# Kernel optimization log

Measured on AMD Instinct MI355X. Metric: run time of the kernel, lower is better.

## Reference

```python
import jax, jax.numpy as jnp
import numpy as np

B, C, D, E = 2048, 64, 1024, 128
P_INT = 0.0  # p_int=0 -> intervention mask is all zeros (deterministic)


def setup_inputs() -> dict:
    key = jax.random.key(0)
    ks = jax.random.split(key, 16)
    s = lambda k, shape, fan: jax.random.normal(k, shape, jnp.float32) * (1.0 / np.sqrt(fan))
    return {
        "x": jax.random.normal(ks[0], (B, D), jnp.float32),
        "c_int": jax.random.uniform(ks[1], (B, C), jnp.float32),
        # stacked per-concept scorer MLP: Linear(D,D) -> ReLU -> Linear(D,1) -> Sigmoid
        "W1": s(ks[2], (C, D, D), D), "b1": jnp.zeros((C, D), jnp.float32),
        "w2": s(ks[3], (C, D), D), "b2": jnp.zeros((C,), jnp.float32),
        # stacked per-concept embed layer: Linear(D+1, D+1) -> ReLU
        "Wl": s(ks[4], (C, D + 1, D + 1), D + 1), "bl": jnp.zeros((C, D + 1), jnp.float32),
        # shared heads
        "Wmu": s(ks[5], (D + 1, E), D + 1), "bmu": jnp.zeros((E,), jnp.float32),
        "Wlv": s(ks[6], (D + 1, E), D + 1), "blv": jnp.zeros((E,), jnp.float32),
        "proto_pos": jax.random.normal(ks[7], (C, E), jnp.float32),
        "proto_neg": jax.random.normal(ks[8], (C, E), jnp.float32),
    }


def reference(x, c_int, W1, b1, w2, b2, Wl, bl, Wmu, bmu, Wlv, blv, proto_pos, proto_neg):
    # Concept scorers (all concepts batched as one grouped GEMM).
    h = jax.nn.relu(jnp.einsum("bd,cdk->bck", x, W1) + b1)          # [B,C,D]
    c_pred = jax.nn.sigmoid(jnp.einsum("bck,ck->bc", h, w2) + b2)    # [B,C]
    # Per-concept embedding layer on [x ; c_pred].
    xc = jnp.concatenate(
        [jnp.broadcast_to(x[:, None, :], (x.shape[0], C, D)), c_pred[..., None]], axis=-1
    )                                                                # [B,C,D+1]
    emb = jax.nn.relu(jnp.einsum("bck,ckj->bcj", xc, Wl) + bl)       # [B,C,D+1]
    mu = jnp.einsum("bcj,je->bce", emb, Wmu) + bmu                   # [B,C,E]
    logvar = jnp.einsum("bcj,je->bce", emb, Wlv) + blv               # [B,C,E]
    c_emb = mu  # eval mode: no reparameterization noise
    # Intervention blend (mask ~ Bernoulli(p_int); p_int=0 -> zeros, deterministic)
    mask = jnp.zeros_like(c_pred)                                    # [B,C]
    cp = mask * c_int + (1.0 - mask) * c_pred                        # [B,C]
    proto = cp[..., None] * proto_pos + (1.0 - cp[..., None]) * proto_neg  # [B,C,E]
    c_emb = mask[..., None] * proto + (1.0 - mask[..., None]) * c_emb
    return (c_pred, c_emb, mu, logvar)
```

## Files before the change

kernel.cpp:

```cpp
#include <hip/hip_runtime.h>
#include <hip/hip_bf16.h>
#include <cstdint>
#include <cstddef>

#define OFF_CE 131072ull
#define OFF_MU (131072ull + 16777216ull)
#define OFF_LV (131072ull + 33554432ull)

using bf16x8 = __attribute__((ext_vector_type(8))) __bf16;
using s16x8  = __attribute__((ext_vector_type(8))) short;
using f32x4  = __attribute__((ext_vector_type(4))) float;

__device__ __forceinline__ unsigned short f2bf(float x) {
  unsigned u = __builtin_bit_cast(unsigned, x);
  return (unsigned short)((u + 0x7FFFu + ((u >> 16) & 1u)) >> 16);
}
__device__ __forceinline__ float bf2f(unsigned short h) {
  unsigned u = ((unsigned)h) << 16;
  return __builtin_bit_cast(float, u);
}
__device__ __forceinline__ void async16(const void* g, void* l) {
  __builtin_amdgcn_global_load_lds(
      (const __attribute__((address_space(1))) void*)g,
      (__attribute__((address_space(3))) void*)l, 16, 0, 0);
}


__global__ __launch_bounds__(256) void convert_x_k(const float* __restrict__ x,
                                                   unsigned short* __restrict__ xb) {
  int idx = blockIdx.x * 256 + threadIdx.x;
  const float4* xv = (const float4*)x;
  float4 a = xv[idx * 2], b = xv[idx * 2 + 1];
  unsigned w0 = f2bf(a.x) | ((unsigned)f2bf(a.y) << 16);
  unsigned w1 = f2bf(a.z) | ((unsigned)f2bf(a.w) << 16);
  unsigned w2 = f2bf(b.x) | ((unsigned)f2bf(b.y) << 16);
  unsigned w3 = f2bf(b.z) | ((unsigned)f2bf(b.w) << 16);
  ((uint4*)xb)[idx] = make_uint4(w0, w1, w2, w3);
}

__global__ void transpose_w1_k(const float* __restrict__ src0, unsigned short* __restrict__ dst0) {
  __shared__ float t[32][33];
  const int c = blockIdx.z;
  const int k0 = blockIdx.x << 5, n0 = blockIdx.y << 5;
  const int tx = threadIdx.x, ty = threadIdx.y;
  const float* src = src0 + ((size_t)c << 20);
#pragma unroll
  for (int r = 0; r < 4; ++r)
    t[ty + (r << 3)][tx] = src[((size_t)(k0 + ty + (r << 3)) << 10) + n0 + tx];
  __syncthreads();
  unsigned short* dst = dst0 + ((size_t)c << 20);
#pragma unroll
  for (int r = 0; r < 4; ++r)
    dst[((size_t)(n0 + ty + (r << 3)) << 10) + k0 + tx] = f2bf(t[tx][ty + (r << 3)]);
}

__global__ void transpose_wl_k(const float* __restrict__ Wl, unsigned short* __restrict__ WlT) {
  __shared__ float t[32][33];
  const int c = blockIdx.z;
  const int k0 = blockIdx.x << 5, n0 = blockIdx.y << 5;
  const int tx = threadIdx.x, ty = threadIdx.y;
  const float* src = Wl + (size_t)c * 1025 * 1025;
#pragma unroll
  for (int r = 0; r < 4; ++r)
    t[ty + (r << 3)][tx] = src[(size_t)(k0 + ty + (r << 3)) * 1025 + n0 + tx];
  __syncthreads();
  unsigned short* dst = WlT + ((size_t)c << 20);
#pragma unroll
  for (int r = 0; r < 4; ++r)
    dst[((size_t)(n0 + ty + (r << 3)) << 10) + k0 + tx] = f2bf(t[tx][ty + (r << 3)]);
}

__global__ __launch_bounds__(256) void prep_wl_k(const float* __restrict__ Wl,
                                                 const float* __restrict__ bl,
                                                 float* __restrict__ wlastf,
                                                 float* __restrict__ blpf,
                                                 float* __restrict__ Wlcolf,
                                                 float* __restrict__ w2l,
                                                 float* __restrict__ bl1024) {
  int idx = blockIdx.x * 256 + threadIdx.x;
  int c = idx >> 10, j = idx & 1023;
  const float* src = Wl + (size_t)c * 1025 * 1025;
  wlastf[idx] = src[(size_t)1024 * 1025 + j];
  blpf[idx]   = bl[(size_t)c * 1025 + j];
  Wlcolf[idx] = src[(size_t)j * 1025 + 1024];
  if (j == 0) {
    w2l[c]    = src[(size_t)1024 * 1025 + 1024];
    bl1024[c] = bl[(size_t)c * 1025 + 1024];
  }
}

__global__ __launch_bounds__(256) void convert_whead_k(const float* __restrict__ Wmu,
                                                       const float* __restrict__ Wlv,
                                                       unsigned short* __restrict__ WheadT,
                                                       float* __restrict__ whead1024f) {
  int idx = blockIdx.x * 256 + threadIdx.x;
  int rr = idx >> 10, k = idx & 1023;
  float v = (rr < 128) ? Wmu[(size_t)k * 128 + rr] : Wlv[(size_t)k * 128 + (rr - 128)];
  WheadT[idx] = f2bf(v);
  if (blockIdx.x == 0 && threadIdx.x < 256) {
    int r2 = threadIdx.x;
    whead1024f[r2] = (r2 < 128) ? Wmu[(size_t)1024 * 128 + r2] : Wlv[(size_t)1024 * 128 + (r2 - 128)];
  }
}

__global__ __launch_bounds__(256) void colgemv_k(const unsigned short* __restrict__ xb,
                                                 const float* __restrict__ Wlcolf,
                                                 float* __restrict__ presum) {
  __shared__ unsigned short xt[32 * 1024];
  const int r0 = blockIdx.x << 5;
  const int tid = threadIdx.x;
#pragma unroll
  for (int i = 0; i < 16; ++i)
    ((uint4*)xt)[tid * 16 + i] = ((const uint4*)(xb + (size_t)r0 * 1024))[tid * 16 + i];
  __syncthreads();
  const int wv = tid >> 6, lane = tid & 63;
  for (int c = 0; c < 64; ++c) {
    float4 w[4];
#pragma unroll
    for (int q = 0; q < 4; ++q)
      w[q] = *(const float4*)(Wlcolf + (c << 10) + lane * 16 + q * 4);
#pragma unroll
    for (int rr = 0; rr < 8; ++rr) {
      const int r = (wv << 3) + rr;
      const unsigned short* xr = xt + (r << 10) + lane * 16;
      s16x8 h0 = *(const s16x8*)xr;
      s16x8 h1 = *(const s16x8*)(xr + 8);
      float s = 0.f;
#pragma unroll
      for (int i = 0; i < 8; ++i) {
        s += bf2f((unsigned short)h0[i]) * ((const float*)&w[i >> 2])[i & 3];
        s += bf2f((unsigned short)h1[i]) * ((const float*)&w[2 + (i >> 2)])[i & 3];
      }
#pragma unroll
      for (int off = 32; off; off >>= 1) s += __shfl_xor(s, off);
      if (lane == 0) presum[(c << 11) + r0 + r] = s;
    }
  }
}

__global__ __launch_bounds__(256) void sigmoid_k(const float* __restrict__ spart,
                                                 const float* __restrict__ b2,
                                                 const float* __restrict__ presum,
                                                 const float* __restrict__ w2l,
                                                 const float* __restrict__ bl1024,
                                                 float* __restrict__ pred_out,
                                                 float* __restrict__ cpf,
                                                 float* __restrict__ e1024f) {
  int idx = blockIdx.x * 256 + threadIdx.x;
  int b = idx >> 6, c = idx & 63;
  float s = b2[c];
#pragma unroll
  for (int q = 0; q < 4; ++q) s += spart[(((size_t)(q << 6) + c) << 11) + b];
  float p = 1.f / (1.f + expf(-s));
  pred_out[idx] = p;
  cpf[idx] = p;
  e1024f[(c << 11) + b] = fmaxf(presum[(c << 11) + b] + p * w2l[c] + bl1024[c], 0.f);
}


#define BAR() __builtin_amdgcn_s_barrier()
#define LGKM0() do { asm volatile("s_waitcnt lgkmcnt(0)" ::: "memory"); \
                     __builtin_amdgcn_sched_barrier(0); } while (0)
#define VM4() asm volatile("s_waitcnt vmcnt(4)" ::: "memory")
#define VM0() asm volatile("s_waitcnt vmcnt(0)" ::: "memory")

#define STAGEA(h, tt, bidx) do { _Pragma("unroll") for (int q_ = 0; q_ < 2; ++q_) \
  async16(Asrc[q_] + ((size_t)(h) * 128) * K + (size_t)(tt) * 64, \
          &sA[bidx][(h) * 8192 + chnk[q_]]); } while (0)
#define STAGEB(h, tt, bidx) do { _Pragma("unroll") for (int q_ = 0; q_ < 2; ++q_) \
  async16(Bsrc[q_] + ((size_t)(h) * 128) * K + (size_t)(tt) * 64, \
          &sB[bidx][(h) * 8192 + chnk[q_]]); } while (0)

#define LOADA(mh, bidx) do { _Pragma("unroll") for (int i_ = 0; i_ < 4; ++i_) { \
  const int ro_ = ((mh) * 128 + wm64 + i_ * 16 + l15) << 6; \
  a[i_][0] = *(const bf16x8*)&sA[bidx][ro_ + ccx0]; \
  a[i_][1] = *(const bf16x8*)&sA[bidx][ro_ + ccx1]; } } while (0)

#define LOADB(nh, bb, bidx) do { _Pragma("unroll") for (int j_ = 0; j_ < 2; ++j_) { \
  const int ro_ = ((nh) * 128 + wn32 + j_ * 16 + l15) << 6; \
  bb[j_][0] = *(const bf16x8*)&sB[bidx][ro_ + ccx0]; \
  bb[j_][1] = *(const bf16x8*)&sB[bidx][ro_ + ccx1]; } } while (0)

#define MMAQ(mh, nh, bb) do { _Pragma("unroll") for (int i_ = 0; i_ < 4; ++i_) \
  _Pragma("unroll") for (int j_ = 0; j_ < 2; ++j_) { \
    acc[(mh)*4+i_][(nh)*2+j_] = __builtin_amdgcn_mfma_f32_16x16x32_bf16( \
        a[i_][0], bb[j_][0], acc[(mh)*4+i_][(nh)*2+j_], 0, 0, 0); \
    acc[(mh)*4+i_][(nh)*2+j_] = __builtin_amdgcn_mfma_f32_16x16x32_bf16( \
        a[i_][1], bb[j_][1], acc[(mh)*4+i_][(nh)*2+j_], 0, 0, 0); \
  } } while (0)

template <int MODE>
__global__ __launch_bounds__(512, 2) void gemm8p_k(
    const unsigned short* __restrict__ A, const unsigned short* __restrict__ BT, const int K,
    const float* __restrict__ e0, const float* __restrict__ e1,
    const float* __restrict__ e2, const float* __restrict__ e3,
    unsigned short* __restrict__ obf, float* __restrict__ ofl) {
  __shared__ unsigned short sA[2][16384];
  __shared__ unsigned short sB[2][16384];

  constexpr int GX = (MODE == 2) ? 1 : 4;
  constexpr int GY = (MODE == 2) ? 512 : 8;
  constexpr int NWG = GX * GY * ((MODE == 2) ? 1 : 64);

  const int tid = threadIdx.x;
  const int lane = tid & 63;
  const int wid = tid >> 6;
  const int wm = wid >> 2, wn = wid & 3;
  const int l15 = lane & 15, l4 = lane >> 4;
  const int wm64 = wm << 6, wn32 = wn << 5;

  const int rbid = blockIdx.x + GX * (blockIdx.y + GY * blockIdx.z);
  const int bid = (rbid & 7) * (NWG >> 3) + (rbid >> 3);
  const int bx = bid % GX;
  const int by = (bid / GX) % GY;
  const int c = bid / (GX * GY);

  const int n0 = bx << 8;
  const int m0 = by << 8;

  const unsigned short* Ab = A;
  const unsigned short* Bb;
  if constexpr (MODE == 2) Bb = BT;
  else                     Bb = BT + ((size_t)c << 20);

  int rloc[2], csrc[2], chnk[2];
  const unsigned short* Asrc[2];
  const unsigned short* Bsrc[2];
#pragma unroll
  for (int q = 0; q < 2; ++q) {
    const int s = ((wid << 1) + q) * 64 + lane;
    rloc[q] = s >> 3;
    csrc[q] = ((s & 7) ^ ((s >> 3) & 7)) << 3;
    chnk[q] = ((wid << 1) + q) << 9;
    Asrc[q] = Ab + (size_t)(m0 + rloc[q]) * K + csrc[q];
    Bsrc[q] = Bb + (size_t)(n0 + rloc[q]) * K + csrc[q];
  }

  const int xorv = l15 & 7;
  const int ccx0 = (l4 ^ xorv) << 3;
  const int ccx1 = ((4 + l4) ^ xorv) << 3;

  f32x4 acc[8][4];
#pragma unroll
  for (int i = 0; i < 8; ++i)
#pragma unroll
    for (int j = 0; j < 4; ++j) acc[i][j] = (f32x4)(0.f);

  bf16x8 a[4][2], b0[2][2], b1[2][2];

  const int nt = K >> 6;

  STAGEA(0, 0, 0); STAGEB(0, 0, 0); STAGEB(1, 0, 0); STAGEA(1, 0, 0);
  VM0();
  BAR();

  for (int t = 0; t < nt - 1; ++t) {
    const int cb = t & 1, nb = cb ^ 1;
    LOADA(0, cb);
    LOADB(0, b0, cb);
    STAGEA(0, t + 1, nb);
    BAR();
    LGKM0();
    __builtin_amdgcn_s_setprio(1);
    MMAQ(0, 0, b0);
    __builtin_amdgcn_s_setprio(0);
    VM4();
    BAR();
    LOADB(1, b1, cb);
    STAGEB(0, t + 1, nb);
    BAR();
    LGKM0();
    __builtin_amdgcn_s_setprio(1);
    MMAQ(0, 1, b1);
    __builtin_amdgcn_s_setprio(0);
    VM4();
    BAR();
    LOADA(1, cb);
    STAGEB(1, t + 1, nb);
    BAR();
    LGKM0();
    __builtin_amdgcn_s_setprio(1);
    MMAQ(1, 1, b1);
    __builtin_amdgcn_s_setprio(0);
    BAR();
    STAGEA(1, t + 1, nb);
    BAR();
    __builtin_amdgcn_s_setprio(1);
    MMAQ(1, 0, b0);
    __builtin_amdgcn_s_setprio(0);
    VM4();
    BAR();
  }

  {
    const int cb = (nt - 1) & 1;
    VM0();
    BAR();
    LOADA(0, cb);
    LOADB(0, b0, cb);
    LGKM0();
    __builtin_amdgcn_s_setprio(1);
    MMAQ(0, 0, b0);
    __builtin_amdgcn_s_setprio(0);
    LOADB(1, b1, cb);
    LGKM0();
    __builtin_amdgcn_s_setprio(1);
    MMAQ(0, 1, b1);
    __builtin_amdgcn_s_setprio(0);
    LOADA(1, cb);
    LGKM0();
    __builtin_amdgcn_s_setprio(1);
    MMAQ(1, 1, b1);
    MMAQ(1, 0, b0);
    __builtin_amdgcn_s_setprio(0);
  }

  int coln[2][2];
#pragma unroll
  for (int nh = 0; nh < 2; ++nh)
#pragma unroll
    for (int j = 0; j < 2; ++j) coln[nh][j] = n0 + nh * 128 + wn32 + j * 16 + l15;

  if constexpr (MODE == 0) {
    float bias[2][2], w2v[2][2];
#pragma unroll
    for (int nh = 0; nh < 2; ++nh)
#pragma unroll
      for (int j = 0; j < 2; ++j) {
        bias[nh][j] = e0[(c << 10) + coln[nh][j]];
        w2v[nh][j]  = e1[(c << 10) + coln[nh][j]];
      }
    float* partL = (float*)&sA[0][0];
#pragma unroll
    for (int mh = 0; mh < 2; ++mh)
#pragma unroll
      for (int i = 0; i < 4; ++i)
#pragma unroll
        for (int rr = 0; rr < 4; ++rr) {
          float s = 0.f;
#pragma unroll
          for (int nh = 0; nh < 2; ++nh)
#pragma unroll
            for (int j = 0; j < 2; ++j) {
              float v = fmaxf(acc[mh * 4 + i][nh * 2 + j][rr] + bias[nh][j], 0.f);
              s += v * w2v[nh][j];
            }
          s += __shfl_xor(s, 1); s += __shfl_xor(s, 2);
          s += __shfl_xor(s, 4); s += __shfl_xor(s, 8);
          if (l15 == 0) partL[wid * 128 + mh * 64 + i * 16 + (l4 << 2) + rr] = s;
        }
    __syncthreads();
    if (tid < 256) {
      const int r = tid;
      const int mh_ = r >> 7, wmr = (r >> 6) & 1, low = r & 63;
      float s2 = 0.f;
#pragma unroll
      for (int wn2 = 0; wn2 < 4; ++wn2) s2 += partL[(wmr * 4 + wn2) * 128 + mh_ * 64 + low];
      ofl[(((size_t)(bx << 6) + c) << 11) + m0 + r] = s2;
    }
  } else if constexpr (MODE == 1) {
    float wl4[2][2], bb4[2][2];
#pragma unroll
    for (int nh = 0; nh < 2; ++nh)
#pragma unroll
      for (int j = 0; j < 2; ++j) {
        wl4[nh][j] = e0[(c << 10) + coln[nh][j]];
        bb4[nh][j] = e1[(c << 10) + coln[nh][j]];
      }
#pragma unroll
    for (int mh = 0; mh < 2; ++mh)
#pragma unroll
      for (int i = 0; i < 4; ++i)
#pragma unroll
        for (int rr = 0; rr < 4; ++rr) {
          const int row = m0 + mh * 128 + wm64 + i * 16 + (l4 << 2) + rr;
          const float cp = e2[((size_t)row << 6) + c];
          unsigned short* orow = obf + (((size_t)(c << 11) + row) << 10);
#pragma unroll
          for (int nh = 0; nh < 2; ++nh)
#pragma unroll
            for (int j = 0; j < 2; ++j) {
              float v = acc[mh * 4 + i][nh * 2 + j][rr] + cp * wl4[nh][j] + bb4[nh][j];
              orow[coln[nh][j]] = f2bf(fmaxf(v, 0.f));
            }
        }
  } else {
    float bias[2][2], wh[2][2];
#pragma unroll
    for (int nh = 0; nh < 2; ++nh)
#pragma unroll
      for (int j = 0; j < 2; ++j) {
        bias[nh][j] = (nh == 0) ? e0[coln[0][j]] : e1[coln[1][j] - 128];
        wh[nh][j]   = e3[coln[nh][j]];
      }
#pragma unroll
    for (int mh = 0; mh < 2; ++mh)
#pragma unroll
      for (int i = 0; i < 4; ++i)
#pragma unroll
        for (int rr = 0; rr < 4; ++rr) {
          const int rid = m0 + mh * 128 + wm64 + i * 16 + (l4 << 2) + rr;
          const int cc = rid >> 11, b = rid & 2047;
          const float ev = e2[rid];
          const size_t ib = (((size_t)b << 6) + cc) << 7;
#pragma unroll
          for (int j = 0; j < 2; ++j) {
            float v = acc[mh * 4 + i][j][rr] + bias[0][j] + ev * wh[0][j];
            ofl[OFF_MU + ib + coln[0][j]] = v;
            ofl[OFF_CE + ib + coln[0][j]] = v;
          }
#pragma unroll
          for (int j = 0; j < 2; ++j) {
            float v = acc[mh * 4 + i][2 + j][rr] + bias[1][j] + ev * wh[1][j];
            ofl[OFF_LV + ib + (coln[1][j] - 128)] = v;
          }
        }
  }
}


extern "C" void kernel_launch(void* const* d_in, const int* in_sizes, int n_in,
                              void* d_out, int out_size, void* d_ws, size_t ws_size,
                              hipStream_t stream) {
  const float* x   = (const float*)d_in[0];
  const float* W1  = (const float*)d_in[2];
  const float* b1  = (const float*)d_in[3];
  const float* w2  = (const float*)d_in[4];
  const float* b2  = (const float*)d_in[5];
  const float* Wl  = (const float*)d_in[6];
  const float* bl  = (const float*)d_in[7];
  const float* Wmu = (const float*)d_in[8];
  const float* bmu = (const float*)d_in[9];
  const float* Wlv = (const float*)d_in[10];
  const float* blv = (const float*)d_in[11];
  float* out = (float*)d_out;

  char* ws = (char*)d_ws;
  unsigned short* xb     = (unsigned short*)(ws);
  unsigned short* WT     = (unsigned short*)(ws + 4194304ull);
  float* wlastf          = (float*)(ws + 138412032ull);
  float* blpf            = (float*)(ws + 138674176ull);
  float* Wlcolf          = (float*)(ws + 138936320ull);
  float* w2l             = (float*)(ws + 139198464ull);
  float* bl1024          = (float*)(ws + 139198720ull);
  unsigned short* WheadT = (unsigned short*)(ws + 139198976ull);
  float* whead1024f      = (float*)(ws + 139723264ull);
  float* presum          = (float*)(ws + 139724288ull);
  float* spart           = (float*)(ws + 140248576ull);
  float* cpf             = (float*)(ws + 142345728ull);
  float* e1024f          = (float*)(ws + 142870016ull);
  unsigned short* emb    = (unsigned short*)(ws + 143394304ull);

  convert_x_k<<<1024, 256, 0, stream>>>(x, xb);
  transpose_w1_k<<<dim3(32, 32, 64), dim3(32, 8), 0, stream>>>(W1, WT);
  prep_wl_k<<<256, 256, 0, stream>>>(Wl, bl, wlastf, blpf, Wlcolf, w2l, bl1024);
  convert_whead_k<<<1024, 256, 0, stream>>>(Wmu, Wlv, WheadT, whead1024f);
  colgemv_k<<<64, 256, 0, stream>>>(xb, Wlcolf, presum);
  gemm8p_k<0><<<dim3(4, 8, 64), 512, 0, stream>>>(xb, WT, 1024, b1, w2, nullptr, nullptr,
                                                  nullptr, spart);
  sigmoid_k<<<512, 256, 0, stream>>>(spart, b2, presum, w2l, bl1024, out, cpf, e1024f);
  transpose_wl_k<<<dim3(32, 32, 64), dim3(32, 8), 0, stream>>>(Wl, WT);
  gemm8p_k<1><<<dim3(4, 8, 64), 512, 0, stream>>>(xb, WT, 1024, wlastf, blpf, cpf, nullptr,
                                                  emb, nullptr);
  gemm8p_k<2><<<dim3(1, 512, 1), 512, 0, stream>>>(emb, WheadT, 1024, bmu, blv, e1024f,
                                                   whead1024f, nullptr, out);
}
```

Before: 1.117 ms.

## Fuse prep kernels and overlap weight transposes with the first grouped GEMM

```diff
diff --git a/kernel.cpp b/kernel.cpp
--- a/kernel.cpp
+++ b/kernel.cpp
@@ -25,136 +25,127 @@
       (__attribute__((address_space(3))) void*)l, 16, 0, 0);
 }
 
-
-__global__ __launch_bounds__(256) void convert_x_k(const float* __restrict__ x,
-                                                   unsigned short* __restrict__ xb) {
-  int idx = blockIdx.x * 256 + threadIdx.x;
-  const float4* xv = (const float4*)x;
-  float4 a = xv[idx * 2], b = xv[idx * 2 + 1];
-  unsigned w0 = f2bf(a.x) | ((unsigned)f2bf(a.y) << 16);
-  unsigned w1 = f2bf(a.z) | ((unsigned)f2bf(a.w) << 16);
-  unsigned w2 = f2bf(b.x) | ((unsigned)f2bf(b.y) << 16);
-  unsigned w3 = f2bf(b.z) | ((unsigned)f2bf(b.w) << 16);
-  ((uint4*)xb)[idx] = make_uint4(w0, w1, w2, w3);
-}
-
-__global__ void transpose_w1_k(const float* __restrict__ src0, unsigned short* __restrict__ dst0) {
-  __shared__ float t[32][33];
-  const int c = blockIdx.z;
-  const int k0 = blockIdx.x << 5, n0 = blockIdx.y << 5;
-  const int tx = threadIdx.x, ty = threadIdx.y;
-  const float* src = src0 + ((size_t)c << 20);
-#pragma unroll
-  for (int r = 0; r < 4; ++r)
-    t[ty + (r << 3)][tx] = src[((size_t)(k0 + ty + (r << 3)) << 10) + n0 + tx];
-  __syncthreads();
-  unsigned short* dst = dst0 + ((size_t)c << 20);
-#pragma unroll
-  for (int r = 0; r < 4; ++r)
-    dst[((size_t)(n0 + ty + (r << 3)) << 10) + k0 + tx] = f2bf(t[tx][ty + (r << 3)]);
-}
-
-__global__ void transpose_wl_k(const float* __restrict__ Wl, unsigned short* __restrict__ WlT) {
-  __shared__ float t[32][33];
-  const int c = blockIdx.z;
-  const int k0 = blockIdx.x << 5, n0 = blockIdx.y << 5;
-  const int tx = threadIdx.x, ty = threadIdx.y;
-  const float* src = Wl + (size_t)c * 1025 * 1025;
-#pragma unroll
-  for (int r = 0; r < 4; ++r)
-    t[ty + (r << 3)][tx] = src[(size_t)(k0 + ty + (r << 3)) * 1025 + n0 + tx];
-  __syncthreads();
-  unsigned short* dst = WlT + ((size_t)c << 20);
-#pragma unroll
-  for (int r = 0; r < 4; ++r)
-    dst[((size_t)(n0 + ty + (r << 3)) << 10) + k0 + tx] = f2bf(t[tx][ty + (r << 3)]);
-}
-
-__global__ __launch_bounds__(256) void prep_wl_k(const float* __restrict__ Wl,
-                                                 const float* __restrict__ bl,
-                                                 float* __restrict__ wlastf,
-                                                 float* __restrict__ blpf,
-                                                 float* __restrict__ Wlcolf,
-                                                 float* __restrict__ w2l,
-                                                 float* __restrict__ bl1024) {
-  int idx = blockIdx.x * 256 + threadIdx.x;
-  int c = idx >> 10, j = idx & 1023;
-  const float* src = Wl + (size_t)c * 1025 * 1025;
-  wlastf[idx] = src[(size_t)1024 * 1025 + j];
-  blpf[idx]   = bl[(size_t)c * 1025 + j];
-  Wlcolf[idx] = src[(size_t)j * 1025 + 1024];
-  if (j == 0) {
-    w2l[c]    = src[(size_t)1024 * 1025 + 1024];
-    bl1024[c] = bl[(size_t)c * 1025 + 1024];
-  }
-}
-
-__global__ __launch_bounds__(256) void convert_whead_k(const float* __restrict__ Wmu,
-                                                       const float* __restrict__ Wlv,
-                                                       unsigned short* __restrict__ WheadT,
-                                                       float* __restrict__ whead1024f) {
-  int idx = blockIdx.x * 256 + threadIdx.x;
-  int rr = idx >> 10, k = idx & 1023;
-  float v = (rr < 128) ? Wmu[(size_t)k * 128 + rr] : Wlv[(size_t)k * 128 + (rr - 128)];
-  WheadT[idx] = f2bf(v);
-  if (blockIdx.x == 0 && threadIdx.x < 256) {
-    int r2 = threadIdx.x;
-    whead1024f[r2] = (r2 < 128) ? Wmu[(size_t)1024 * 128 + r2] : Wlv[(size_t)1024 * 128 + (r2 - 128)];
-  }
-}
-
-__global__ __launch_bounds__(256) void colgemv_k(const unsigned short* __restrict__ xb,
-                                                 const float* __restrict__ Wlcolf,
-                                                 float* __restrict__ presum) {
-  __shared__ unsigned short xt[32 * 1024];
-  const int r0 = blockIdx.x << 5;
+struct P {
+  const float *Wl, *bl, *Wmu, *Wlv, *b2;
+  const unsigned short *xb;
+  unsigned short *WlT, *WheadT;
+  float *wlastf, *blpf, *Wlcolf, *w2l, *bl1024, *whead1024f, *presum, *spart, *e1024, *pred;
+};
+
+__device__ __forceinline__ void strip_transpose(const float* __restrict__ srcBase, int srcStride,
+                                                unsigned short* __restrict__ dstBase, int tid,
+                                                char* lds) {
+  float* t64 = (float*)lds;
+  const int r = tid >> 3;
+  const int c8 = (tid & 7) << 3;
+  for (int nc = 0; nc < 16; ++nc) {
+    __syncthreads();
+    const float* sp = srcBase + (size_t)r * srcStride + nc * 64 + c8;
+#pragma unroll
+    for (int j = 0; j < 8; ++j) t64[r * 65 + c8 + j] = sp[j];
+    __syncthreads();
+    unsigned short tmp[8];
+#pragma unroll
+    for (int j = 0; j < 8; ++j) tmp[j] = f2bf(t64[(c8 + j) * 65 + r]);
+    *(uint4*)(dstBase + (size_t)(nc * 64 + r) * 1024 + c8) = *(uint4*)tmp;
+  }
+}
+
+__global__ __launch_bounds__(512) void prep1_k(const float* __restrict__ W1,
+                                               const float* __restrict__ x,
+                                               const float* __restrict__ Wl,
+                                               const float* __restrict__ bl,
+                                               unsigned short* __restrict__ xb,
+                                               unsigned short* __restrict__ W1T,
+                                               float* __restrict__ wlastf,
+                                               float* __restrict__ blpf,
+                                               float* __restrict__ Wlcolf,
+                                               float* __restrict__ w2l,
+                                               float* __restrict__ bl1024) {
+  __shared__ char lds[16640];
+  const int bid = blockIdx.x;
   const int tid = threadIdx.x;
-#pragma unroll
-  for (int i = 0; i < 16; ++i)
-    ((uint4*)xt)[tid * 16 + i] = ((const uint4*)(xb + (size_t)r0 * 1024))[tid * 16 + i];
+  if (bid < 1024) {
+    const int c = bid & 63, k0 = (bid >> 6) << 6;
+    strip_transpose(W1 + ((size_t)c << 20) + (size_t)k0 * 1024, 1024,
+                    W1T + ((size_t)c << 20) + k0, tid, lds);
+  } else if (bid < 1536) {
+    const int idx = (bid - 1024) * 512 + tid;
+    const float4* xv = (const float4*)x;
+    float4 a = xv[idx * 2], b = xv[idx * 2 + 1];
+    unsigned w0 = f2bf(a.x) | ((unsigned)f2bf(a.y) << 16);
+    unsigned w1 = f2bf(a.z) | ((unsigned)f2bf(a.w) << 16);
+    unsigned w2 = f2bf(b.x) | ((unsigned)f2bf(b.y) << 16);
+    unsigned w3 = f2bf(b.z) | ((unsigned)f2bf(b.w) << 16);
+    ((uint4*)xb)[idx] = make_uint4(w0, w1, w2, w3);
+  } else {
+    const int idx = (bid - 1536) * 512 + tid;
+    const int c = idx >> 10, j = idx & 1023;
+    const float* src = Wl + (size_t)c * 1050625;
+    wlastf[idx] = src[(size_t)1024 * 1025 + j];
+    blpf[idx]   = bl[(size_t)c * 1025 + j];
+    Wlcolf[idx] = src[(size_t)j * 1025 + 1024];
+    if (j == 0) {
+      w2l[c]    = src[(size_t)1024 * 1025 + 1024];
+      bl1024[c] = bl[(size_t)c * 1025 + 1024];
+    }
+  }
+}
+
+__global__ __launch_bounds__(512) void transpose_wl_strip_k(const float* __restrict__ Wl,
+                                                            unsigned short* __restrict__ WlT) {
+  __shared__ char lds[16640];
+  const int bid = blockIdx.x;
+  const int c = bid & 63, k0 = (bid >> 6) << 6;
+  strip_transpose(Wl + (size_t)c * 1050625 + (size_t)k0 * 1025, 1025,
+                  WlT + ((size_t)c << 20) + k0, threadIdx.x, lds);
+}
+
+template <int FUSE_WL>
+__device__ void extra_work(int e, int tid, char* lds, const P& p) {
+  if constexpr (FUSE_WL) {
+    if (e < 1024) {
+      const int c = e & 63, k0 = (e >> 6) << 6;
+      strip_transpose(p.Wl + (size_t)c * 1050625 + (size_t)k0 * 1025, 1025,
+                      p.WlT + ((size_t)c << 20) + k0, tid, lds);
+      return;
+    }
+    e -= 1024;
+  }
+  if (e < 512) {
+    const int idx = e * 512 + tid;
+    const int rr = idx >> 10, k = idx & 1023;
+    float v = (rr < 128) ? p.Wmu[(size_t)k * 128 + rr] : p.Wlv[(size_t)k * 128 + (rr - 128)];
+    p.WheadT[idx] = f2bf(v);
+    if (e == 0 && tid < 256)
+      p.whead1024f[tid] = (tid < 128) ? p.Wmu[131072 + tid] : p.Wlv[131072 + (tid - 128)];
+    return;
+  }
+  e -= 512;
+  const int r0 = e << 5;
+  uint4* xt4 = (uint4*)lds;
+  const uint4* src4 = (const uint4*)(p.xb + ((size_t)r0 << 10));
+#pragma unroll
+  for (int i = 0; i < 8; ++i) xt4[tid * 8 + i] = src4[tid * 8 + i];
   __syncthreads();
   const int wv = tid >> 6, lane = tid & 63;
+  const unsigned short* xt = (const unsigned short*)lds;
   for (int c = 0; c < 64; ++c) {
-    float4 w[4];
-#pragma unroll
-    for (int q = 0; q < 4; ++q)
-      w[q] = *(const float4*)(Wlcolf + (c << 10) + lane * 16 + q * 4);
-#pragma unroll
-    for (int rr = 0; rr < 8; ++rr) {
-      const int r = (wv << 3) + rr;
+    float w[16];
+#pragma unroll
+    for (int q = 0; q < 16; ++q) w[q] = p.Wlcolf[(c << 10) + lane * 16 + q];
+#pragma unroll
+    for (int rr = 0; rr < 4; ++rr) {
+      const int r = (wv << 2) + rr;
       const unsigned short* xr = xt + (r << 10) + lane * 16;
-      s16x8 h0 = *(const s16x8*)xr;
-      s16x8 h1 = *(const s16x8*)(xr + 8);
       float s = 0.f;
 #pragma unroll
-      for (int i = 0; i < 8; ++i) {
-        s += bf2f((unsigned short)h0[i]) * ((const float*)&w[i >> 2])[i & 3];
-        s += bf2f((unsigned short)h1[i]) * ((const float*)&w[2 + (i >> 2)])[i & 3];
-      }
+      for (int i = 0; i < 16; ++i) s += bf2f(xr[i]) * w[i];
 #pragma unroll
       for (int off = 32; off; off >>= 1) s += __shfl_xor(s, off);
-      if (lane == 0) presum[(c << 11) + r0 + r] = s;
+      if (lane == 0) p.presum[(c << 11) + r0 + r] = s;
     }
   }
-}
-
-__global__ __launch_bounds__(256) void sigmoid_k(const float* __restrict__ spart,
-                                                 const float* __restrict__ b2,
-                                                 const float* __restrict__ presum,
-                                                 const float* __restrict__ w2l,
-                                                 const float* __restrict__ bl1024,
-                                                 float* __restrict__ pred_out,
-                                                 float* __restrict__ cpf,
-                                                 float* __restrict__ e1024f) {
-  int idx = blockIdx.x * 256 + threadIdx.x;
-  int b = idx >> 6, c = idx & 63;
-  float s = b2[c];
-#pragma unroll
-  for (int q = 0; q < 4; ++q) s += spart[(((size_t)(q << 6) + c) << 11) + b];
-  float p = 1.f / (1.f + expf(-s));
-  pred_out[idx] = p;
-  cpf[idx] = p;
-  e1024f[(c << 11) + b] = fmaxf(presum[(c << 11) + b] + p * w2l[c] + bl1024[c], 0.f);
 }
 
 
@@ -189,12 +180,12 @@
         a[i_][1], bb[j_][1], acc[(mh)*4+i_][(nh)*2+j_], 0, 0, 0); \
   } } while (0)
 
-template <int MODE>
+template <int MODE, int FUSE_WL>
 __global__ __launch_bounds__(512, 2) void gemm8p_k(
     const unsigned short* __restrict__ A, const unsigned short* __restrict__ BT, const int K,
     const float* __restrict__ e0, const float* __restrict__ e1,
     const float* __restrict__ e2, const float* __restrict__ e3,
-    unsigned short* __restrict__ obf, float* __restrict__ ofl) {
+    unsigned short* __restrict__ obf, float* __restrict__ ofl, P p) {
   __shared__ unsigned short sA[2][16384];
   __shared__ unsigned short sB[2][16384];
 
@@ -203,13 +194,26 @@
   constexpr int NWG = GX * GY * ((MODE == 2) ? 1 : 64);
 
   const int tid = threadIdx.x;
+
+  int rbid;
+  if constexpr (MODE == 0) {
+    constexpr int NE = FUSE_WL ? 1600 : 576;
+    constexpr int NT = 2048 + NE;
+    const int bidR = blockIdx.x;
+    const int lo = (int)(((long)bidR * NE) / NT);
+    const int hi = (int)(((long)(bidR + 1) * NE) / NT);
+    if (hi > lo) { extra_work<FUSE_WL>(lo, tid, (char*)&sA[0][0], p); return; }
+    rbid = bidR - lo;
+  } else {
+    rbid = blockIdx.x + GX * (blockIdx.y + GY * blockIdx.z);
+  }
+
   const int lane = tid & 63;
   const int wid = tid >> 6;
   const int wm = wid >> 2, wn = wid & 3;
   const int l15 = lane & 15, l4 = lane >> 4;
   const int wm64 = wm << 6, wn32 = wn << 5;
 
-  const int rbid = blockIdx.x + GX * (blockIdx.y + GY * blockIdx.z);
   const int bid = (rbid & 7) * (NWG >> 3) + (rbid >> 3);
   const int bx = bid % GX;
   const int by = (bid / GX) % GY;
@@ -359,6 +363,21 @@
       ofl[(((size_t)(bx << 6) + c) << 11) + m0 + r] = s2;
     }
   } else if constexpr (MODE == 1) {
+    float* cpL = (float*)&sA[0][0];
+    if (tid < 256) {
+      const int b = m0 + tid;
+      float s = p.b2[c];
+#pragma unroll
+      for (int q = 0; q < 4; ++q) s += e2[(((size_t)(q << 6) + c) << 11) + b];
+      float pv = 1.f / (1.f + expf(-s));
+      cpL[tid] = pv;
+      if (bx == 0) {
+        p.pred[((size_t)b << 6) + c] = pv;
+        p.e1024[(c << 11) + b] =
+            fmaxf(p.presum[(c << 11) + b] + pv * p.w2l[c] + p.bl1024[c], 0.f);
+      }
+    }
+    __syncthreads();
     float wl4[2][2], bb4[2][2];
 #pragma unroll
     for (int nh = 0; nh < 2; ++nh)
@@ -373,8 +392,9 @@
       for (int i = 0; i < 4; ++i)
 #pragma unroll
         for (int rr = 0; rr < 4; ++rr) {
-          const int row = m0 + mh * 128 + wm64 + i * 16 + (l4 << 2) + rr;
-          const float cp = e2[((size_t)row << 6) + c];
+          const int rl = mh * 128 + wm64 + i * 16 + (l4 << 2) + rr;
+          const int row = m0 + rl;
+          const float cp = cpL[rl];
           unsigned short* orow = obf + (((size_t)(c << 11) + row) << 10);
 #pragma unroll
           for (int nh = 0; nh < 2; ++nh)
@@ -435,33 +455,44 @@
   const float* blv = (const float*)d_in[11];
   float* out = (float*)d_out;
 
+  const bool fuse = ws_size >= 545523712ull;
+
   char* ws = (char*)d_ws;
-  unsigned short* xb     = (unsigned short*)(ws);
-  unsigned short* WT     = (unsigned short*)(ws + 4194304ull);
-  float* wlastf          = (float*)(ws + 138412032ull);
-  float* blpf            = (float*)(ws + 138674176ull);
-  float* Wlcolf          = (float*)(ws + 138936320ull);
-  float* w2l             = (float*)(ws + 139198464ull);
-  float* bl1024          = (float*)(ws + 139198720ull);
-  unsigned short* WheadT = (unsigned short*)(ws + 139198976ull);
-  float* whead1024f      = (float*)(ws + 139723264ull);
-  float* presum          = (float*)(ws + 139724288ull);
-  float* spart           = (float*)(ws + 140248576ull);
-  float* cpf             = (float*)(ws + 142345728ull);
-  float* e1024f          = (float*)(ws + 142870016ull);
-  unsigned short* emb    = (unsigned short*)(ws + 143394304ull);
-
-  convert_x_k<<<1024, 256, 0, stream>>>(x, xb);
-  transpose_w1_k<<<dim3(32, 32, 64), dim3(32, 8), 0, stream>>>(W1, WT);
-  prep_wl_k<<<256, 256, 0, stream>>>(Wl, bl, wlastf, blpf, Wlcolf, w2l, bl1024);
-  convert_whead_k<<<1024, 256, 0, stream>>>(Wmu, Wlv, WheadT, whead1024f);
-  colgemv_k<<<64, 256, 0, stream>>>(xb, Wlcolf, presum);
-  gemm8p_k<0><<<dim3(4, 8, 64), 512, 0, stream>>>(xb, WT, 1024, b1, w2, nullptr, nullptr,
-                                                  nullptr, spart);
-  sigmoid_k<<<512, 256, 0, stream>>>(spart, b2, presum, w2l, bl1024, out, cpf, e1024f);
-  transpose_wl_k<<<dim3(32, 32, 64), dim3(32, 8), 0, stream>>>(Wl, WT);
-  gemm8p_k<1><<<dim3(4, 8, 64), 512, 0, stream>>>(xb, WT, 1024, wlastf, blpf, cpf, nullptr,
-                                                  emb, nullptr);
-  gemm8p_k<2><<<dim3(1, 512, 1), 512, 0, stream>>>(emb, WheadT, 1024, bmu, blv, e1024f,
-                                                   whead1024f, nullptr, out);
-}
+  size_t off = 0;
+  auto take = [&](size_t bytes) { char* r = ws + off; off += bytes; return r; };
+  unsigned short* xb     = (unsigned short*)take(4194304);
+  unsigned short* W1T    = (unsigned short*)take(134217728);
+  unsigned short* WlT    = fuse ? (unsigned short*)take(134217728) : W1T;
+  float* wlastf          = (float*)take(262144);
+  float* blpf            = (float*)take(262144);
+  float* Wlcolf          = (float*)take(262144);
+  float* w2l             = (float*)take(512);
+  float* bl1024          = (float*)take(512);
+  unsigned short* WheadT = (unsigned short*)take(524288);
+  float* whead1024f      = (float*)take(1024);
+  float* presum          = (float*)take(524288);
+  float* spart           = (float*)take(2097152);
+  float* e1024f          = (float*)take(524288);
+  unsigned short* emb    = (unsigned short*)take(268435456);
+
+  P p;
+  p.Wl = Wl; p.bl = bl; p.Wmu = Wmu; p.Wlv = Wlv; p.b2 = b2;
+  p.xb = xb; p.WlT = WlT; p.WheadT = WheadT;
+  p.wlastf = wlastf; p.blpf = blpf; p.Wlcolf = Wlcolf; p.w2l = w2l; p.bl1024 = bl1024;
+  p.whead1024f = whead1024f; p.presum = presum; p.spart = spart;
+  p.e1024 = e1024f; p.pred = out;
+
+  prep1_k<<<1664, 512, 0, stream>>>(W1, x, Wl, bl, xb, W1T, wlastf, blpf, Wlcolf, w2l, bl1024);
+  if (fuse) {
+    gemm8p_k<0, 1><<<2048 + 1600, 512, 0, stream>>>(xb, W1T, 1024, b1, w2, nullptr, nullptr,
+                                                    nullptr, spart, p);
+  } else {
+    gemm8p_k<0, 0><<<2048 + 576, 512, 0, stream>>>(xb, W1T, 1024, b1, w2, nullptr, nullptr,
+                                                   nullptr, spart, p);
+    transpose_wl_strip_k<<<1024, 512, 0, stream>>>(Wl, WlT);
+  }
+  gemm8p_k<1, 0><<<dim3(4, 8, 64), 512, 0, stream>>>(xb, WlT, 1024, wlastf, blpf, spart, nullptr,
+                                                     emb, nullptr, p);
+  gemm8p_k<2, 0><<<dim3(1, 512, 1), 512, 0, stream>>>(emb, WheadT, 1024, bmu, blv, e1024f,
+                                                      whead1024f, nullptr, out, p);
+}
```

Result: no change. 1.137 ms (+1.8%).
